# Kernel tuning notes

Measured on AMD Instinct MI355X. Metric: run time of the kernel, lower is better.

## Reference

```python
import jax, jax.numpy as jnp
import numpy as np
from jax import lax

PATCH_SIZE = 14
BLUR_W_L, BLUR_PAD_L, BLUR_REPEATS_L = 5, 2, 5
BLUR_W_U, BLUR_PAD_U, BLUR_REPEATS_U = 7, 3, 3
TOPK_RATIO = 0.001
EPS = 1e-12


def setup_inputs() -> dict:
    key = jax.random.key(0)
    k1, k2, k3, k4 = jax.random.split(key, 4)
    B, N, C = 16, 1024, 768  # 448/14 = 32 -> 32*32 = 1024 patches
    return {
        "middle_patch": jax.random.normal(k1, (B, N, C), dtype=jnp.float32),
        "last_patch": jax.random.normal(k2, (B, N, C), dtype=jnp.float32),
        "predicted_middle_patch": jax.random.normal(k3, (B, N, C), dtype=jnp.float32),
        "predicted_last_patch": jax.random.normal(k4, (B, N, C), dtype=jnp.float32),
        "out_h": 448,
        "out_w": 448,
    }


def _l2_normalize(x):
    # matches torch F.normalize(dim=-1): x / max(||x||_2, 1e-12)
    n = jnp.sqrt(jnp.sum(x * x, axis=-1, keepdims=True))
    return x / jnp.maximum(n, EPS)


def _conv_blur(x, k, pad):
    # x: (B,1,H,W); uniform kxk box filter, stride 1, same-size output
    w = jnp.full((1, 1, k, k), 1.0 / (k * k), dtype=x.dtype)
    return lax.conv_general_dilated(
        x, w, window_strides=(1, 1), padding=[(pad, pad), (pad, pad)],
        dimension_numbers=("NCHW", "OIHW", "NCHW"))


def _blur(x):
    for _ in range(BLUR_REPEATS_L):
        x = _conv_blur(x, BLUR_W_L, BLUR_PAD_L)
    for _ in range(BLUR_REPEATS_U):
        x = _conv_blur(x, BLUR_W_U, BLUR_PAD_U)
    return x


def reference(middle_patch, last_patch, predicted_middle_patch,
              predicted_last_patch, out_h, out_w):
    b = middle_patch.shape[0]
    h, w = int(out_h), int(out_w)
    h_p, w_p = h // PATCH_SIZE, w // PATCH_SIZE

    middle_anom = jnp.sqrt(jnp.sum(
        (_l2_normalize(predicted_middle_patch) - _l2_normalize(middle_patch)) ** 2, axis=-1))
    last_anom = jnp.sqrt(jnp.sum(
        (_l2_normalize(predicted_last_patch) - _l2_normalize(last_patch)) ** 2, axis=-1))
    combined = middle_anom * last_anom  # (B, h_p*w_p)

    anomaly_map = combined.reshape(b, 1, h_p, w_p)
    # bilinear upsample with half-pixel centers == torch align_corners=False
    anomaly_map = jax.image.resize(anomaly_map, (b, 1, h, w), method="bilinear")
    anomaly_map = _blur(anomaly_map)

    n = h * w
    k = max(1, int(n * TOPK_RATIO))
    topk_vals, _ = lax.top_k(anomaly_map.reshape(b, n), k)
    pred_score = jnp.mean(topk_vals, axis=1)
    return anomaly_map, pred_score
```

## Files before the change

### kernel.cpp

```cpp
#include <hip/hip_runtime.h>

constexpr int C = 768;
constexpr int NPATCH = 1024;
constexpr int H = 448, W = 448;
constexpr int HW = H * W;
constexpr int TOPK = 200;
constexpr float EPS = 1e-12f;

constexpr int HBITS = 13;
constexpr int HBINS = 1 << HBITS;
constexpr int HSHIFT = 18;
constexpr int SLICES = 32;
constexpr int CSTRIDE = 64;

typedef float f32x4 __attribute__((ext_vector_type(4)));

__device__ __forceinline__ float dotv(const f32x4 a, const f32x4 b) {
    return a.x * b.x + a.y * b.y + a.z * b.z + a.w * b.w;
}

__global__ __launch_bounds__(256, 4) void anom_kernel(
    const float* __restrict__ m, const float* __restrict__ l,
    const float* __restrict__ pm, const float* __restrict__ pl,
    float* __restrict__ combined, int rows) {
    int wid = (int)((blockIdx.x * blockDim.x + threadIdx.x) >> 6);
    int lane = threadIdx.x & 63;
    if (wid >= rows) return;
    size_t base = (size_t)wid * C;
    const f32x4* A = (const f32x4*)(m + base);
    const f32x4* B = (const f32x4*)(pm + base);
    const f32x4* Cc = (const f32x4*)(l + base);
    const f32x4* D = (const f32x4*)(pl + base);

    f32x4 a0 = __builtin_nontemporal_load(A + lane);
    f32x4 a1 = __builtin_nontemporal_load(A + lane + 64);
    f32x4 a2 = __builtin_nontemporal_load(A + lane + 128);
    f32x4 b0 = __builtin_nontemporal_load(B + lane);
    f32x4 b1 = __builtin_nontemporal_load(B + lane + 64);
    f32x4 b2 = __builtin_nontemporal_load(B + lane + 128);
    f32x4 c0 = __builtin_nontemporal_load(Cc + lane);
    f32x4 c1 = __builtin_nontemporal_load(Cc + lane + 64);
    f32x4 c2 = __builtin_nontemporal_load(Cc + lane + 128);
    f32x4 d0 = __builtin_nontemporal_load(D + lane);
    f32x4 d1 = __builtin_nontemporal_load(D + lane + 64);
    f32x4 d2 = __builtin_nontemporal_load(D + lane + 128);

    float mm = dotv(a0, a0) + dotv(a1, a1) + dotv(a2, a2);
    float pp = dotv(b0, b0) + dotv(b1, b1) + dotv(b2, b2);
    float mp = dotv(a0, b0) + dotv(a1, b1) + dotv(a2, b2);
    float ll = dotv(c0, c0) + dotv(c1, c1) + dotv(c2, c2);
    float qq = dotv(d0, d0) + dotv(d1, d1) + dotv(d2, d2);
    float lq = dotv(c0, d0) + dotv(c1, d1) + dotv(c2, d2);

#pragma unroll
    for (int off = 32; off > 0; off >>= 1) {
        mm += __shfl_xor(mm, off);
        pp += __shfl_xor(pp, off);
        mp += __shfl_xor(mp, off);
        ll += __shfl_xor(ll, off);
        qq += __shfl_xor(qq, off);
        lq += __shfl_xor(lq, off);
    }
    if (lane == 0) {
        float rm = 1.0f / fmaxf(sqrtf(mm), EPS);
        float rp = 1.0f / fmaxf(sqrtf(pp), EPS);
        float rl = 1.0f / fmaxf(sqrtf(ll), EPS);
        float rq = 1.0f / fmaxf(sqrtf(qq), EPS);
        float d2m = fmaxf(mm * rm * rm - 2.f * mp * rm * rp + pp * rp * rp, 0.f);
        float d2l = fmaxf(ll * rl * rl - 2.f * lq * rl * rq + qq * rq * rq, 0.f);
        combined[wid] = sqrtf(d2m) * sqrtf(d2l);
    }
}


__global__ __launch_bounds__(512) void gmat_kernel(float* __restrict__ G) {
    __shared__ float g[32][449];
    int tid = threadIdx.x;
    int i = tid & 31;
    int chunk = tid >> 5;
    int x0 = chunk * 28;

#pragma unroll 1
    for (int k = 0; k < 28; ++k) {
        int x = x0 + k;
        float sx = (x + 0.5f) * (1.0f / 14.0f) - 0.5f;
        float f0 = floorf(sx);
        float fx = sx - f0;
        int q0 = (int)f0;
        int q0c = min(max(q0, 0), 31);
        int q1c = min(max(q0 + 1, 0), 31);
        float w = 0.f;
        if (q0c == i) w += 1.0f - fx;
        if (q1c == i) w += fx;
        g[i][x] = w;
    }
    __syncthreads();

#pragma unroll 1
    for (int pass = 0; pass < 8; ++pass) {
        float win[34];
#pragma unroll
        for (int j = 0; j < 34; ++j) {
            int xw = x0 - 3 + j;
            win[j] = (xw >= 0 && xw < 448) ? g[i][xw] : 0.f;
        }
        float out[28];
        if (pass < 5) {
            constexpr float inv5 = 1.0f / 5.0f;
#pragma unroll
            for (int k = 0; k < 28; ++k)
                out[k] = (win[k + 1] + win[k + 2] + win[k + 3] + win[k + 4] +
                          win[k + 5]) * inv5;
        } else {
            constexpr float inv7 = 1.0f / 7.0f;
#pragma unroll
            for (int k = 0; k < 28; ++k)
                out[k] = (win[k] + win[k + 1] + win[k + 2] + win[k + 3] +
                          win[k + 4] + win[k + 5] + win[k + 6]) * inv7;
        }
        __syncthreads();
#pragma unroll
        for (int k = 0; k < 28; ++k) g[i][x0 + k] = out[k];
        __syncthreads();
    }
#pragma unroll
    for (int k = 0; k < 28; ++k) G[(x0 + k) * 32 + i] = g[i][x0 + k];
}

__global__ __launch_bounds__(448) void stageA_kernel(
    const float* __restrict__ comb, const float* __restrict__ G,
    float* __restrict__ T) {
    __shared__ float combT[32][32];
    int b = blockIdx.x;
    int x = threadIdx.x;
    const float* cb = comb + (size_t)b * 1024;
    for (int idx = x; idx < 1024; idx += 448)
        combT[idx & 31][idx >> 5] = cb[idx];

    f32x4 grow[8];
#pragma unroll
    for (int k = 0; k < 8; ++k)
        grow[k] = *(const f32x4*)(G + x * 32 + k * 4);
    f32x4 acc[8];
#pragma unroll
    for (int k = 0; k < 8; ++k) acc[k] = (f32x4){0.f, 0.f, 0.f, 0.f};
    __syncthreads();
#pragma unroll
    for (int j = 0; j < 32; ++j) {
        float w = grow[j >> 2][j & 3];
#pragma unroll
        for (int k = 0; k < 8; ++k) {
            f32x4 c = *(const f32x4*)&combT[j][k * 4];
            acc[k] += c * w;
        }
    }
    float* t = T + ((size_t)b * 448 + x) * 32;
#pragma unroll
    for (int k = 0; k < 8; ++k) *(f32x4*)(t + k * 4) = acc[k];
}

__global__ __launch_bounds__(448) void stageB_kernel(
    const float* __restrict__ T, const float* __restrict__ G,
    float* __restrict__ map) {
    __shared__ float gl[448 * 36];
    int b = blockIdx.x >> 4;
    int band = blockIdx.x & 15;
    int x = threadIdx.x;
#pragma unroll
    for (int k = 0; k < 8; ++k)
        *(f32x4*)&gl[x * 36 + k * 4] = *(const f32x4*)(G + x * 32 + k * 4);
    f32x4 t[8];
    const float* tp = T + ((size_t)b * 448 + x) * 32;
#pragma unroll
    for (int k = 0; k < 8; ++k) t[k] = *(const f32x4*)(tp + k * 4);
    __syncthreads();

    float* out = map + (size_t)b * HW + (size_t)band * 28 * W;
#pragma unroll 1
    for (int yy = 0; yy < 28; ++yy) {
        int y = band * 28 + yy;
        f32x4 a = {0.f, 0.f, 0.f, 0.f};
#pragma unroll
        for (int k = 0; k < 8; ++k) {
            f32x4 g4 = *(const f32x4*)&gl[y * 36 + k * 4];
            a += g4 * t[k];
        }
        out[yy * W + x] = a.x + a.y + a.z + a.w;
    }
}


__global__ __launch_bounds__(256) void zero4_kernel(uint4* __restrict__ p,
                                                    int n4) {
    int i = blockIdx.x * blockDim.x + threadIdx.x;
    if (i < n4) p[i] = make_uint4(0u, 0u, 0u, 0u);
}

__global__ __launch_bounds__(256) void hist_kernel(
    const float* __restrict__ map, unsigned* __restrict__ hist) {
    __shared__ unsigned lh[HBINS];
    int b = blockIdx.x / SLICES, sl = blockIdx.x % SLICES;
    for (int i = threadIdx.x; i < HBINS; i += 256) lh[i] = 0;
    __syncthreads();
    const uint4* u4 = (const uint4*)(map + (size_t)b * HW);
    int per4 = HW / SLICES / 4;
    int start = sl * per4;
    for (int i = start + threadIdx.x; i < start + per4; i += 256) {
        uint4 v = u4[i];
        atomicAdd(&lh[v.x >> HSHIFT], 1u);
        atomicAdd(&lh[v.y >> HSHIFT], 1u);
        atomicAdd(&lh[v.z >> HSHIFT], 1u);
        atomicAdd(&lh[v.w >> HSHIFT], 1u);
    }
    __syncthreads();
    unsigned* gh = hist + (size_t)b * HBINS;
    for (int i = threadIdx.x; i < HBINS; i += 256) {
        unsigned c = lh[i];
        if (c) atomicAdd(&gh[i], c);
    }
}

__global__ __launch_bounds__(256) void select_kernel(
    const unsigned* __restrict__ hist, int* __restrict__ selbin) {
    int b = blockIdx.x;
    const unsigned* gh = hist + (size_t)b * HBINS;
    constexpr int CHUNK = HBINS / 256;
    __shared__ unsigned ss[257];
    __shared__ unsigned cs2[33];
    __shared__ int sh_base, sh_k;
    int tid = threadIdx.x;
    unsigned s = 0;
#pragma unroll
    for (int j = 0; j < CHUNK; ++j) s += gh[tid * CHUNK + j];
    ss[tid] = s;
    if (tid == 0) ss[256] = 0;
    __syncthreads();
#pragma unroll
    for (int st = 1; st < 256; st <<= 1) {
        unsigned add = (tid + st < 256) ? ss[tid + st] : 0u;
        __syncthreads();
        ss[tid] += add;
        __syncthreads();
    }
    if ((int)ss[tid] >= TOPK && (int)ss[tid + 1] < TOPK) {
        sh_base = tid * CHUNK;
        sh_k = TOPK - (int)ss[tid + 1];
    }
    __syncthreads();
    int base = sh_base, kk = sh_k;
    if (tid < 32) cs2[tid] = gh[base + tid];
    if (tid == 0) cs2[32] = 0;
    __syncthreads();
#pragma unroll
    for (int st = 1; st < 32; st <<= 1) {
        unsigned add = (tid < 32 && tid + st < 32) ? cs2[tid + st] : 0u;
        __syncthreads();
        if (tid < 32) cs2[tid] += add;
        __syncthreads();
    }
    if (tid < 32 && (int)cs2[tid] >= kk && (int)cs2[tid + 1] < kk)
        selbin[b * CSTRIDE] = base + tid;
}

__global__ __launch_bounds__(256) void compact_kernel(
    const float* __restrict__ map, const int* __restrict__ selbin,
    int* __restrict__ ccount, float* __restrict__ cand) {
    int tid = threadIdx.x;
    size_t base = (size_t)blockIdx.x * 1024;
    int b = (int)(base / HW);
    int sb = selbin[b * CSTRIDE];
    const uint4* u4 = (const uint4*)(((const unsigned*)map) + base);
    uint4 v = u4[tid];
    unsigned take0 = ((int)(v.x >> HSHIFT) >= sb);
    unsigned take1 = ((int)(v.y >> HSHIFT) >= sb);
    unsigned take2 = ((int)(v.z >> HSHIFT) >= sb);
    unsigned take3 = ((int)(v.w >> HSHIFT) >= sb);
    int c = (int)(take0 + take1 + take2 + take3);

    __shared__ int blkcnt, blkbase;
    if (tid == 0) blkcnt = 0;
    __syncthreads();
    int pos = 0;
    if (c) pos = atomicAdd(&blkcnt, c);
    __syncthreads();
    if (tid == 0 && blkcnt > 0)
        blkbase = atomicAdd(&ccount[b * CSTRIDE], blkcnt);
    __syncthreads();
    if (c) {
        float* o = cand + (size_t)b * HW + blkbase + pos;
        if (take0) *o++ = __uint_as_float(v.x);
        if (take1) *o++ = __uint_as_float(v.y);
        if (take2) *o++ = __uint_as_float(v.z);
        if (take3) *o = __uint_as_float(v.w);
    }
}

__global__ __launch_bounds__(256) void topk_kernel(
    const float* __restrict__ cand, const int* __restrict__ ccount,
    float* __restrict__ score) {
    int b = blockIdx.x;
    const float* s = cand + (size_t)b * HW;
    const unsigned* u = (const unsigned*)s;
    int M = ccount[b * CSTRIDE];
    __shared__ unsigned hist[256];
    __shared__ unsigned ss[257];
    __shared__ unsigned sh_prefix;
    __shared__ int sh_k;
    int tid = threadIdx.x;

    unsigned prefix = 0;
    int k = TOPK;
    for (int dgt = 3; dgt >= 0; --dgt) {
        hist[tid] = 0;
        __syncthreads();
        for (int i = tid; i < M; i += 256) {
            unsigned v = u[i];
            bool match = (dgt == 3) || ((v >> (8 * (dgt + 1))) == prefix);
            if (match) atomicAdd(&hist[(v >> (8 * dgt)) & 255u], 1u);
        }
        __syncthreads();
        ss[tid] = hist[tid];
        if (tid == 0) ss[256] = 0;
        __syncthreads();
#pragma unroll
        for (int st = 1; st < 256; st <<= 1) {
            unsigned add = (tid + st < 256) ? ss[tid + st] : 0u;
            __syncthreads();
            ss[tid] += add;
            __syncthreads();
        }
        if ((int)ss[tid] >= k && (int)ss[tid + 1] < k) {
            sh_prefix = (prefix << 8) | (unsigned)tid;
            sh_k = k - (int)ss[tid + 1];
        }
        __syncthreads();
        prefix = sh_prefix;
        k = sh_k;
        __syncthreads();
    }

    float thr = __uint_as_float(prefix);
    float sum = 0.f;
    int cnt = 0;
    for (int i = tid; i < M; i += 256) {
        float v = s[i];
        if (v > thr) { sum += v; cnt++; }
    }
#pragma unroll
    for (int off = 32; off > 0; off >>= 1) {
        sum += __shfl_xor(sum, off);
        cnt += __shfl_xor(cnt, off);
    }
    __shared__ float wsum[4];
    __shared__ int wcnt[4];
    int wv = tid >> 6;
    if ((tid & 63) == 0) { wsum[wv] = sum; wcnt[wv] = cnt; }
    __syncthreads();
    if (tid == 0) {
        float s2 = 0.f;
        int c2 = 0;
        for (int i = 0; i < 4; ++i) { s2 += wsum[i]; c2 += wcnt[i]; }
        score[b] = (s2 + (float)(TOPK - c2) * thr) * (1.0f / TOPK);
    }
}

extern "C" void kernel_launch(void* const* d_in, const int* in_sizes, int n_in,
                              void* d_out, int out_size, void* d_ws, size_t ws_size,
                              hipStream_t stream) {
    const float* mid = (const float*)d_in[0];
    const float* last = (const float*)d_in[1];
    const float* pmid = (const float*)d_in[2];
    const float* plast = (const float*)d_in[3];
    int B = in_sizes[0] / (NPATCH * C);

    float* out_map = (float*)d_out;
    float* out_score = out_map + (size_t)B * HW;

    float* combined = (float*)d_ws;
    int* meta = (int*)((char*)d_ws + 64 * 1024);
    int* ccount = meta;
    int* selbin = meta + 16 * CSTRIDE;
    unsigned* hist = (unsigned*)((char*)d_ws + 72 * 1024);
    float* Gw = (float*)((char*)d_ws + 584 * 1024);
    float* Tw = (float*)((char*)d_ws + 644 * 1024);
    float* cand = (float*)((char*)d_ws + 1540 * 1024);

    int n4 = (520 * 1024) / 16;
    zero4_kernel<<<(n4 + 255) / 256, 256, 0, stream>>>(
        (uint4*)((char*)d_ws + 64 * 1024), n4);

    gmat_kernel<<<1, 512, 0, stream>>>(Gw);

    int rows = B * NPATCH;
    anom_kernel<<<(rows + 3) / 4, 256, 0, stream>>>(mid, last, pmid, plast,
                                                    combined, rows);

    stageA_kernel<<<B, 448, 0, stream>>>(combined, Gw, Tw);
    stageB_kernel<<<B * 16, 448, 0, stream>>>(Tw, Gw, out_map);

    hist_kernel<<<B * SLICES, 256, 0, stream>>>(out_map, hist);
    select_kernel<<<B, 256, 0, stream>>>(hist, selbin);
    int nc = (B * HW) / 1024;
    compact_kernel<<<nc, 256, 0, stream>>>(out_map, selbin, ccount, cand);
    topk_kernel<<<B, 256, 0, stream>>>(cand, ccount, out_score);
}
```

Measured before the change: 110.4 us.

## Fuse histogram into stageB and merge zeroing with G-matrix init

The histogram pass is folded into stageB, so each output value is binned into a shared-memory histogram as soon as it is written, removing a separate full re-read of the map. The zeroing kernel is merged into the G-matrix kernel as extra blocks, saving one launch. stageB now loads only its 28-row band of G into shared memory instead of all 448 rows. The cost is shared atomics and a 32KB local histogram per stageB block, which may lower occupancy, plus more global atomic merges (256 blocks instead of 512, so actually fewer).

```diff
diff --git a/kernel.cpp b/kernel.cpp
--- a/kernel.cpp
+++ b/kernel.cpp
@@ -10,7 +10,6 @@
 constexpr int HBITS = 13;
 constexpr int HBINS = 1 << HBITS;
 constexpr int HSHIFT = 18;
-constexpr int SLICES = 32;
 constexpr int CSTRIDE = 64;
 
 typedef float f32x4 __attribute__((ext_vector_type(4)));
@@ -73,7 +72,14 @@
 }
 
 
-__global__ __launch_bounds__(512) void gmat_kernel(float* __restrict__ G) {
+__global__ __launch_bounds__(512) void init_kernel(float* __restrict__ G,
+                                                   uint4* __restrict__ zp,
+                                                   int n4) {
+    if (blockIdx.x != 0) {
+        int i = (blockIdx.x - 1) * 512 + threadIdx.x;
+        if (i < n4) zp[i] = make_uint4(0u, 0u, 0u, 0u);
+        return;
+    }
     __shared__ float g[32][449];
     int tid = threadIdx.x;
     int i = tid & 31;
@@ -161,14 +167,16 @@
 
 __global__ __launch_bounds__(448) void stageB_kernel(
     const float* __restrict__ T, const float* __restrict__ G,
-    float* __restrict__ map) {
-    __shared__ float gl[448 * 36];
+    float* __restrict__ map, unsigned* __restrict__ hist) {
+    __shared__ float gband[28][32];
+    __shared__ unsigned lh[HBINS];
     int b = blockIdx.x >> 4;
     int band = blockIdx.x & 15;
     int x = threadIdx.x;
-#pragma unroll
-    for (int k = 0; k < 8; ++k)
-        *(f32x4*)&gl[x * 36 + k * 4] = *(const f32x4*)(G + x * 32 + k * 4);
+
+    for (int i = x; i < HBINS; i += 448) lh[i] = 0;
+    for (int i = x; i < 28 * 32; i += 448)
+        gband[i >> 5][i & 31] = G[(band * 28 + (i >> 5)) * 32 + (i & 31)];
     f32x4 t[8];
     const float* tp = T + ((size_t)b * 448 + x) * 32;
 #pragma unroll
@@ -178,47 +186,24 @@
     float* out = map + (size_t)b * HW + (size_t)band * 28 * W;
 #pragma unroll 1
     for (int yy = 0; yy < 28; ++yy) {
-        int y = band * 28 + yy;
         f32x4 a = {0.f, 0.f, 0.f, 0.f};
 #pragma unroll
         for (int k = 0; k < 8; ++k) {
-            f32x4 g4 = *(const f32x4*)&gl[y * 36 + k * 4];
+            f32x4 g4 = *(const f32x4*)&gband[yy][k * 4];
             a += g4 * t[k];
         }
-        out[yy * W + x] = a.x + a.y + a.z + a.w;
-    }
-}
-
-
-__global__ __launch_bounds__(256) void zero4_kernel(uint4* __restrict__ p,
-                                                    int n4) {
-    int i = blockIdx.x * blockDim.x + threadIdx.x;
-    if (i < n4) p[i] = make_uint4(0u, 0u, 0u, 0u);
-}
-
-__global__ __launch_bounds__(256) void hist_kernel(
-    const float* __restrict__ map, unsigned* __restrict__ hist) {
-    __shared__ unsigned lh[HBINS];
-    int b = blockIdx.x / SLICES, sl = blockIdx.x % SLICES;
-    for (int i = threadIdx.x; i < HBINS; i += 256) lh[i] = 0;
-    __syncthreads();
-    const uint4* u4 = (const uint4*)(map + (size_t)b * HW);
-    int per4 = HW / SLICES / 4;
-    int start = sl * per4;
-    for (int i = start + threadIdx.x; i < start + per4; i += 256) {
-        uint4 v = u4[i];
-        atomicAdd(&lh[v.x >> HSHIFT], 1u);
-        atomicAdd(&lh[v.y >> HSHIFT], 1u);
-        atomicAdd(&lh[v.z >> HSHIFT], 1u);
-        atomicAdd(&lh[v.w >> HSHIFT], 1u);
+        float v = a.x + a.y + a.z + a.w;
+        out[yy * W + x] = v;
+        atomicAdd(&lh[__float_as_uint(v) >> HSHIFT], 1u);
     }
     __syncthreads();
     unsigned* gh = hist + (size_t)b * HBINS;
-    for (int i = threadIdx.x; i < HBINS; i += 256) {
+    for (int i = x; i < HBINS; i += 448) {
         unsigned c = lh[i];
         if (c) atomicAdd(&gh[i], c);
     }
 }
+
 
 __global__ __launch_bounds__(256) void select_kernel(
     const unsigned* __restrict__ hist, int* __restrict__ selbin) {
@@ -386,19 +371,16 @@
     float* cand = (float*)((char*)d_ws + 1540 * 1024);
 
     int n4 = (520 * 1024) / 16;
-    zero4_kernel<<<(n4 + 255) / 256, 256, 0, stream>>>(
-        (uint4*)((char*)d_ws + 64 * 1024), n4);
-
-    gmat_kernel<<<1, 512, 0, stream>>>(Gw);
+    init_kernel<<<1 + (n4 + 511) / 512, 512, 0, stream>>>(
+        Gw, (uint4*)((char*)d_ws + 64 * 1024), n4);
 
     int rows = B * NPATCH;
     anom_kernel<<<(rows + 3) / 4, 256, 0, stream>>>(mid, last, pmid, plast,
                                                     combined, rows);
 
     stageA_kernel<<<B, 448, 0, stream>>>(combined, Gw, Tw);
-    stageB_kernel<<<B * 16, 448, 0, stream>>>(Tw, Gw, out_map);
-
-    hist_kernel<<<B * SLICES, 256, 0, stream>>>(out_map, hist);
+    stageB_kernel<<<B * 16, 448, 0, stream>>>(Tw, Gw, out_map, hist);
+
     select_kernel<<<B, 256, 0, stream>>>(hist, selbin);
     int nc = (B * HW) / 1024;
     compact_kernel<<<nc, 256, 0, stream>>>(out_map, selbin, ccount, cand);
```

Result: faster. 100.6 us (-8.9%).
